# Optimization experiments

Measured on AMD Instinct MI355X. Metric: run time of the kernel, lower is better.

Reference implementation:

```python
import jax, jax.numpy as jnp
import numpy as np

B, S = 64, 256
F, H, V = 512, 2048, 32000
PAD = 0
LN_EPS = 1e-5


def setup_inputs() -> dict:
    key = jax.random.key(0)
    ks = jax.random.split(key, 10)
    inputs = jax.random.randint(ks[0], (B, S), 0, V, dtype=jnp.int64)
    targets = jax.random.randint(ks[1], (B, S), 0, V, dtype=jnp.int64)
    # parameters (kaiming-ish / torch-default-ish scales)
    see = jax.random.normal(ks[2], (2 * F, F), jnp.float32) * (2.0 / (2 * F)) ** 0.5
    bias = jnp.zeros((F,), jnp.float32)
    W_in = jax.random.normal(ks[3], (H, F), jnp.float32) * (1.0 / F) ** 0.5
    b_in = jnp.zeros((H,), jnp.float32)
    W_out = jax.random.normal(ks[4], (F, H), jnp.float32) * (1.0 / H) ** 0.5
    b_out = jnp.zeros((F,), jnp.float32)
    ln_g = jnp.ones((F,), jnp.float32)
    ln_b = jnp.zeros((F,), jnp.float32)
    emb = jax.random.normal(ks[5], (V, F), jnp.float32)
    return {"inputs": inputs, "targets": targets, "see": see, "bias": bias,
            "W_in": W_in, "b_in": b_in, "W_out": W_out, "b_out": b_out,
            "ln_g": ln_g, "ln_b": ln_b, "emb": emb}


def _layernorm(x, g, b):
    mu = jnp.mean(x, axis=-1, keepdims=True)
    var = jnp.mean((x - mu) ** 2, axis=-1, keepdims=True)
    return (x - mu) * jax.lax.rsqrt(var + LN_EPS) * g + b


def reference(inputs, targets, see, bias, W_in, b_in, W_out, b_out, ln_g, ln_b, emb):
    emb_m = emb.at[PAD].set(0.0)  # padding_idx row is zero
    inv_sqrt_f = 1.0 / (F ** 0.5)

    def step(state, xy):
        idx, tgt = xy                      # [B], [B]
        vecs = emb_m[idx]                  # [B,F]
        gate = jax.nn.sigmoid(jnp.concatenate([vecs, state], axis=-1) @ see + bias)
        cont = state * gate + vecs * (1.0 - gate)
        h = jax.nn.relu(_layernorm(cont, ln_g, ln_b) @ W_in.T + b_in)
        out = h @ W_out.T + b_out          # [B,F]
        logits = (out @ emb_m.T) * inv_sqrt_f  # [B,V]
        logp = jax.nn.log_softmax(logits, axis=-1)
        nll = -jnp.take_along_axis(logp, tgt[:, None], axis=1)[:, 0]
        mask = (tgt != PAD).astype(logits.dtype)
        li = jnp.sum(nll * mask) / jnp.maximum(jnp.sum(mask), 1.0)
        return cont, li

    xs = (inputs.T, targets.T)  # [S,B]
    _, losses = jax.lax.scan(step, jnp.zeros((inputs.shape[0], F), emb.dtype), xs)
    return jnp.mean(losses)
```

## Files before the change

### kernel.cpp

```cpp
#include <hip/hip_runtime.h>
#include <hip/hip_fp8.h>

#define F_DIM 512
#define H_DIM 2048
#define V_DIM 32000
#define B_DIM 64
#define S_DIM 256
#define ROWS (S_DIM*B_DIM)
#define NT_LOG 250
#define SCALE 0.04419417382415922f
#define LSE_OFF 40.0f

typedef __attribute__((ext_vector_type(8))) short  short8;
typedef __attribute__((ext_vector_type(4))) float  floatx4;

static __device__ inline unsigned short f2bf(float x){
  unsigned int u = __float_as_uint(x);
  u += 0x7fffu + ((u >> 16) & 1u);
  return (unsigned short)(u >> 16);
}
static __device__ inline float bf2f(unsigned short u){
  return __uint_as_float(((unsigned int)u) << 16);
}
static __device__ inline unsigned char f2fp8(float x){
  __hip_fp8_e4m3 q(x);
  return q.__x;
}
static __device__ inline int sw8(int row, int col){
  int g = (col >> 3) & 7;
  int chunk = ((g >> 1) ^ ((row >> 1) & 3));
  int lob = (g & 1) ^ ((row >> 3) & 1);
  return (col & ~63) | (chunk << 4) | (lob << 3) | (col & 7);
}
static __device__ inline float wsum(float v){
  #pragma unroll
  for(int m = 32; m > 0; m >>= 1) v += __shfl_xor(v, m);
  return v;
}
static __device__ inline void load_lds16(const void* g, void* l){
  __builtin_amdgcn_global_load_lds((const __attribute__((address_space(1))) void*)g,
                                   (__attribute__((address_space(3))) void*)l, 16, 0, 0);
}

__global__ __launch_bounds__(256) void cast_w(const float* __restrict__ src,
                                              unsigned short* __restrict__ dst, int n){
  int i = blockIdx.x*256 + threadIdx.x;
  int stride = gridDim.x*256;
  for(; i < n; i += stride) dst[i] = f2bf(src[i]);
}
__global__ __launch_bounds__(256) void cast_emb(const float* __restrict__ src,
    unsigned short* __restrict__ dst, unsigned char* __restrict__ d8){
  int i = blockIdx.x*256 + threadIdx.x;
  int stride = gridDim.x*256;
  for(; i < V_DIM*F_DIM; i += stride){
    float v = (i < F_DIM) ? 0.f : src[i];
    dst[i] = f2bf(v);
    int row = i >> 9, col = i & 511;
    d8[(long)row*512 + sw8(row, col)] = f2fp8(v);
  }
}

__global__ __launch_bounds__(256) void prep_see(const float* __restrict__ see,
    unsigned short* __restrict__ TT, unsigned char* __restrict__ B8){
  int n = blockIdx.x;
  for(int k = threadIdx.x; k < 512; k += 256){
    TT[n*512 + k] = f2bf(see[(long)k*512 + n]);
    B8[n*512 + k] = f2fp8(see[(long)(512+k)*512 + n]);
  }
}

__global__ __launch_bounds__(256) void gather_vecs(const float* __restrict__ emb,
    const int* __restrict__ inp, unsigned short* __restrict__ V){
  long row = (long)blockIdx.x*4 + (threadIdx.x >> 6);
  int l = threadIdx.x & 63;
  int t = (int)(row >> 6), b = (int)(row & 63);
  int idx = inp[b*S_DIM + t];
  short8 o;
  if (idx == 0){
    #pragma unroll
    for(int i=0;i<8;i++) o[i] = 0;
  } else {
    const float* e = emb + (long)idx*F_DIM + l*8;
    float4 a = *(const float4*)e;
    float4 bq = *(const float4*)(e + 4);
    o[0]=(short)f2bf(a.x); o[1]=(short)f2bf(a.y); o[2]=(short)f2bf(a.z); o[3]=(short)f2bf(a.w);
    o[4]=(short)f2bf(bq.x);o[5]=(short)f2bf(bq.y);o[6]=(short)f2bf(bq.z);o[7]=(short)f2bf(bq.w);
  }
  *(short8*)(V + row*F_DIM + l*8) = o;
}

__global__ __launch_bounds__(512, 1) void recurrence_batch(
    const unsigned int* __restrict__ ZV,
    const unsigned char* __restrict__ W8,
    unsigned short* __restrict__ CONTB)
{
  __shared__ unsigned char stt[2][16][520];

  const int tid = threadIdx.x;
  const int w  = tid >> 6;
  const int l  = tid & 63;
  const int rl = l & 15, rq = l >> 4;
  const int wg = blockIdx.x;
  const int colb = w*64;

  long Bfr[16][4];
  #pragma unroll
  for(int c=0;c<16;c++)
    #pragma unroll
    for(int tl=0;tl<4;tl++)
      Bfr[c][tl] = *(const long*)(W8 + (long)(colb + tl*16 + rl)*512 + c*32 + rq*8);

  float s_old[16];
  #pragma unroll
  for(int i=0;i<16;i++) s_old[i] = 0.f;

  const unsigned int* zbase = ZV + (long)(wg*16 + rq*4)*512 + colb + rl;
  unsigned short* cbase = CONTB + ((long)wg*16 + rq*4)*512 + colb + rl;

  unsigned int zv[16];
  #pragma unroll
  for(int tl=0;tl<4;tl++)
    #pragma unroll
    for(int r=0;r<4;r++)
      zv[tl*4+r] = zbase[(long)r*512 + tl*16];

  for(int t = 0; t < S_DIM; t++){
    unsigned int zvn[16];
    if (t+1 < S_DIM){
      const unsigned int* zp = zbase + (long)(t+1)*64*512;
      #pragma unroll
      for(int tl=0;tl<4;tl++)
        #pragma unroll
        for(int r=0;r<4;r++)
          zvn[tl*4+r] = zp[(long)r*512 + tl*16];
    }

    asm volatile("s_waitcnt lgkmcnt(0)" ::: "memory");
    __builtin_amdgcn_s_barrier();
    asm volatile("" ::: "memory");

    floatx4 acc[4];
    #pragma unroll
    for(int tl=0;tl<4;tl++) acc[tl] = (floatx4)0.f;

    if (t > 0){
      const unsigned char* sb = &stt[(t-1)&1][0][0];
      #pragma unroll
      for(int c=0;c<16;c++){
        long a = *(const long*)(sb + rl*520 + c*32 + rq*8);
        #pragma unroll
        for(int tl=0;tl<4;tl++)
          acc[tl] = __builtin_amdgcn_mfma_f32_16x16x32_fp8_fp8(a, Bfr[c][tl], acc[tl], 0, 0, 0);
      }
    }

    unsigned short* cw = cbase + (long)t*64*512;
    unsigned char* swb = &stt[t&1][0][0] + rq*4*520 + colb + rl;
    #pragma unroll
    for(int tl=0;tl<4;tl++){
      float sv[4];
      #pragma unroll
      for(int r=0;r<4;r++){
        unsigned int p = zv[tl*4+r];
        float z = __uint_as_float(p << 16) + acc[tl][r];
        float v = __uint_as_float(p & 0xffff0000u);
        float e = __expf(-z);
        float g = __builtin_amdgcn_rcpf(1.f + e);
        float s = fmaf(s_old[tl*4+r] - v, g, v);
        s_old[tl*4+r] = s;
        sv[r] = s;
      }
      #pragma unroll
      for(int pr=0; pr<2; pr++){
        unsigned int bfp, f8p;
        asm("v_cvt_pk_bf16_f32 %0, %1, %2" : "=v"(bfp) : "v"(sv[pr*2]), "v"(sv[pr*2+1]));
        asm("v_cvt_pk_fp8_f32 %0, %1, %2"  : "=v"(f8p) : "v"(sv[pr*2]), "v"(sv[pr*2+1]));
        cw[(long)(pr*2)*512   + tl*16] = (unsigned short)(bfp & 0xffffu);
        cw[(long)(pr*2+1)*512 + tl*16] = (unsigned short)(bfp >> 16);
        swb[(pr*2)*520   + tl*16] = (unsigned char)(f8p & 0xffu);
        swb[(pr*2+1)*520 + tl*16] = (unsigned char)((f8p >> 8) & 0xffu);
      }
    }

    if (t+1 < S_DIM){
      #pragma unroll
      for(int i=0;i<16;i++) zv[i] = zvn[i];
    }
  }
}

__global__ __launch_bounds__(256) void ln_kernel(const unsigned short* __restrict__ contb,
    const float* __restrict__ lg, const float* __restrict__ lb,
    unsigned short* __restrict__ xln)
{
  const int wid = threadIdx.x >> 6, l = threadIdx.x & 63;
  const long row = (long)blockIdx.x*4 + wid;
  short8 xv = *(const short8*)(contb + row*F_DIM + l*8);
  float v[8];
  #pragma unroll
  for(int i=0;i<8;i++) v[i] = bf2f((unsigned short)xv[i]);
  float s = 0.f;
  #pragma unroll
  for(int i=0;i<8;i++) s += v[i];
  s = wsum(s);
  float mu = s * (1.f/512.f);
  float q = 0.f;
  #pragma unroll
  for(int i=0;i<8;i++){ float d = v[i]-mu; q += d*d; }
  q = wsum(q);
  float rs = rsqrtf(q*(1.f/512.f) + 1e-5f);
  short8 o;
  #pragma unroll
  for(int i=0;i<8;i++)
    o[i] = (short)f2bf((v[i]-mu)*rs*lg[l*8+i] + lb[l*8+i]);
  *(short8*)(xln + row*F_DIM + l*8) = o;
}

template<int MODE>
__global__ __launch_bounds__(256) void gemm_bt(
    const unsigned short* __restrict__ A,
    const unsigned short* __restrict__ Bm,
    const float* __restrict__ bias,
    unsigned short* __restrict__ C,
    unsigned char* __restrict__ C8,
    const unsigned short* __restrict__ Vsrc,
    unsigned int* __restrict__ ZVout,
    int M, int N, int K, int tiles_m, int tiles_n)
{
  __shared__ short As[128*64];
  __shared__ short Bs[128*64];

  const int bid = blockIdx.x;
  const int mt = bid % tiles_m;
  const int nt = bid / tiles_m;
  const long m0 = (long)mt * 128;
  const long n0 = (long)nt * 128;
  const int tid = threadIdx.x;
  const int l = tid & 63;
  const int wid = tid >> 6;
  const int wr = wid >> 1, wc = wid & 1;
  const int rl = l & 15, rq = l >> 4;

  const short* Ag = (const short*)A + m0 * K;
  const short* Bg = (const short*)Bm + n0 * K;
  const int grow = tid >> 3;
  const int kp = tid & 7;
  const int ksw = (kp ^ (grow & 7)) * 8;

  floatx4 acc[4][4];
  #pragma unroll
  for(int i=0;i<4;i++)
    #pragma unroll
    for(int j=0;j<4;j++) acc[i][j] = (floatx4)0.f;

  for(int k0 = 0; k0 < K; k0 += 64){
    __syncthreads();
    #pragma unroll
    for(int ro = 0; ro < 128; ro += 32){
      load_lds16(Ag + (long)(ro + grow)*K + k0 + ksw, (void*)(As + (ro+grow)*64 + kp*8));
      load_lds16(Bg + (long)(ro + grow)*K + k0 + ksw, (void*)(Bs + (ro+grow)*64 + kp*8));
    }
    __syncthreads();
    #pragma unroll
    for(int kb = 0; kb < 64; kb += 32){
      const int cb = kb >> 3;
      const int cl = ((cb + rq) ^ (rl & 7)) * 8;
      short8 af[4], bfr[4];
      #pragma unroll
      for(int i=0;i<4;i++) af[i]  = *(const short8*)(As + (wr*64 + i*16 + rl)*64 + cl);
      #pragma unroll
      for(int j=0;j<4;j++) bfr[j] = *(const short8*)(Bs + (wc*64 + j*16 + rl)*64 + cl);
      #pragma unroll
      for(int i=0;i<4;i++)
        #pragma unroll
        for(int j=0;j<4;j++)
          acc[i][j] = __builtin_amdgcn_mfma_f32_16x16x32_bf16(af[i], bfr[j], acc[i][j], 0, 0, 0);
    }
  }

  const long mb = m0 + wr*64;
  const long nb = n0 + wc*64;
  #pragma unroll
  for(int j=0;j<4;j++){
    float bj = bias[nb + j*16 + rl];
    #pragma unroll
    for(int i=0;i<4;i++){
      #pragma unroll
      for(int r=0;r<4;r++){
        float v = acc[i][j][r] + bj;
        if (MODE == 0) v = fmaxf(v, 0.f);
        int rowI = (int)(mb + i*16 + rq*4 + r);
        int colI = (int)(nb + j*16 + rl);
        long idx = (long)rowI*N + colI;
        if (MODE == 5){
          ZVout[idx] = ((unsigned)Vsrc[idx] << 16) | (unsigned)f2bf(v);
        } else {
          C[idx] = f2bf(v);
          if (MODE == 4) C8[(long)rowI*512 + sw8(rowI, colI)] = f2fp8(v);
        }
      }
    }
  }
}

__global__ __launch_bounds__(256) void gemm_f8_logits(
    const unsigned char* __restrict__ A8,
    const unsigned char* __restrict__ B8,
    float* __restrict__ part,
    int M, int N, int K, int tiles_m, int tiles_n)
{
  __shared__ unsigned char As8[128*64];
  __shared__ unsigned char Bs8[128*64];
  __shared__ float sm2[2][64][2];

  const int bid = blockIdx.x;
  const int mt = bid % tiles_m;
  const int nt = bid / tiles_m;
  const long m0 = (long)mt * 128;
  const long n0 = (long)nt * 128;
  const int tid = threadIdx.x;
  const int l = tid & 63;
  const int wid = tid >> 6;
  const int wr = wid >> 1, wc = wid & 1;
  const int rl = l & 15, rq = l >> 4;

  const unsigned char* Ag = A8 + m0 * K;
  const unsigned char* Bg = B8 + n0 * K;
  const int grow = tid >> 2;
  const int kp = tid & 3;

  floatx4 acc[4][4];
  #pragma unroll
  for(int i=0;i<4;i++)
    #pragma unroll
    for(int j=0;j<4;j++) acc[i][j] = (floatx4)0.f;

  const int rsw = (rl >> 1) & 3;
  const int rhi = (rl >> 3) & 1;

  for(int k0 = 0; k0 < K; k0 += 64){
    __syncthreads();
    #pragma unroll
    for(int ro = 0; ro < 128; ro += 64){
      load_lds16(Ag + (long)(ro + grow)*K + k0 + kp*16, (void*)(As8 + (ro+grow)*64 + kp*16));
      load_lds16(Bg + (long)(ro + grow)*K + k0 + kp*16, (void*)(Bs8 + (ro+grow)*64 + kp*16));
    }
    __syncthreads();
    #pragma unroll
    for(int kb = 0; kb < 64; kb += 32){
      const int g = (kb >> 3) + rq;
      const int cl = ((((g >> 1) ^ rsw)) << 4) | ((((g & 1) ^ rhi)) << 3);
      long af[4], bfr[4];
      #pragma unroll
      for(int i=0;i<4;i++) af[i]  = *(const long*)(As8 + (wr*64 + i*16 + rl)*64 + cl);
      #pragma unroll
      for(int j=0;j<4;j++) bfr[j] = *(const long*)(Bs8 + (wc*64 + j*16 + rl)*64 + cl);
      #pragma unroll
      for(int i=0;i<4;i++)
        #pragma unroll
        for(int j=0;j<4;j++)
          acc[i][j] = __builtin_amdgcn_mfma_f32_16x16x32_fp8_fp8(af[i], bfr[j], acc[i][j], 0, 0, 0);
    }
  }

  #pragma unroll
  for(int i=0;i<4;i++){
    #pragma unroll
    for(int r=0;r<4;r++){
      float sv = 0.f;
      #pragma unroll
      for(int j=0;j<4;j++) sv += __expf(acc[i][j][r]*SCALE - LSE_OFF);
      #pragma unroll
      for(int d=1; d<16; d<<=1) sv += __shfl_xor(sv, d);
      if (rl == 0) sm2[wr][i*16 + rq*4 + r][wc] = sv;
    }
  }
  __syncthreads();
  if (tid < 128){
    int wr2 = tid >> 6, rowl = tid & 63;
    part[(m0 + wr2*64 + rowl)*tiles_n + nt] = sm2[wr2][rowl][0] + sm2[wr2][rowl][1];
  }
}

__global__ __launch_bounds__(256) void tlogit_kernel(const unsigned short* __restrict__ outb,
    const unsigned short* __restrict__ embb, const int* __restrict__ tgt,
    float* __restrict__ TL)
{
  long gw = (long)blockIdx.x*4 + (threadIdx.x >> 6);
  int l = threadIdx.x & 63;
  int t = (int)(gw >> 6), b = (int)(gw & 63);
  int tg = tgt[b*S_DIM + t];
  const unsigned short* o = outb + gw*F_DIM;
  const unsigned short* e = embb + (long)tg*F_DIM;
  short8 ov = *(const short8*)(o + l*8);
  short8 ev = *(const short8*)(e + l*8);
  float s = 0.f;
  #pragma unroll
  for(int i=0;i<8;i++) s += bf2f((unsigned short)ov[i]) * bf2f((unsigned short)ev[i]);
  s = wsum(s);
  if (l == 0) TL[gw] = s * SCALE;
}

__global__ __launch_bounds__(256) void lse_kernel(const float* __restrict__ part,
    const float* __restrict__ TL, float* __restrict__ nll)
{
  long row = (long)blockIdx.x*4 + (threadIdx.x >> 6);
  int l = threadIdx.x & 63;
  float S = 0.f;
  for(int c = l; c < NT_LOG; c += 64)
    S += part[row*NT_LOG + c];
  S = wsum(S);
  if (l == 0) nll[row] = (LSE_OFF + logf(S)) - TL[row];
}

__global__ __launch_bounds__(256) void loss_kernel(const float* __restrict__ nll,
    const int* __restrict__ tgt, float* __restrict__ out)
{
  int t = threadIdx.x;
  float s = 0.f; int cnt = 0;
  for(int b = 0; b < B_DIM; b++){
    int v = tgt[b*S_DIM + t];
    if (v != 0){ s += nll[(long)t*B_DIM + b]; cnt++; }
  }
  float li = s / fmaxf((float)cnt, 1.f);
  li = wsum(li);
  __shared__ float red[4];
  if ((t & 63) == 0) red[t >> 6] = li;
  __syncthreads();
  if (t == 0) out[0] = (red[0]+red[1]+red[2]+red[3]) * (1.f/256.f);
}

extern "C" void kernel_launch(void* const* d_in, const int* in_sizes, int n_in,
                              void* d_out, int out_size, void* d_ws, size_t ws_size,
                              hipStream_t stream)
{
  const int*   inp   = (const int*)d_in[0];
  const int*   tgt   = (const int*)d_in[1];
  const float* see   = (const float*)d_in[2];
  const float* bias  = (const float*)d_in[3];
  const float* W_in  = (const float*)d_in[4];
  const float* b_in  = (const float*)d_in[5];
  const float* W_out = (const float*)d_in[6];
  const float* b_out = (const float*)d_in[7];
  const float* ln_g  = (const float*)d_in[8];
  const float* ln_b  = (const float*)d_in[9];
  const float* emb   = (const float*)d_in[10];

  char* p = (char*)d_ws;
  unsigned short* CONTB= (unsigned short*)p; p += (size_t)ROWS*F_DIM*2;
  unsigned short* Hb   = (unsigned short*)p; p += (size_t)ROWS*H_DIM*2;
  unsigned short* OUTb = (unsigned short*)p; p += (size_t)ROWS*F_DIM*2;
  unsigned short* EMBb = (unsigned short*)p; p += (size_t)V_DIM*F_DIM*2;
  unsigned char* EMB8  = (unsigned char*)p;  p += (size_t)V_DIM*F_DIM;
  unsigned short* WINb = (unsigned short*)p; p += (size_t)H_DIM*F_DIM*2;
  unsigned short* WOUTb= (unsigned short*)p; p += (size_t)F_DIM*H_DIM*2;
  float* TL            = (float*)p;          p += (size_t)ROWS*4;
  float* NLL           = (float*)p;          p += (size_t)ROWS*4;
  unsigned short* VECSb= (unsigned short*)p; p += (size_t)ROWS*F_DIM*2;
  unsigned int* ZV     = (unsigned int*)p;   p += (size_t)ROWS*F_DIM*4;
  unsigned short* SEETT= (unsigned short*)p; p += (size_t)F_DIM*F_DIM*2;
  unsigned char* SEEB8 = (unsigned char*)p;  p += (size_t)F_DIM*F_DIM;
  unsigned short* XLN  = (unsigned short*)ZV;
  unsigned char* OUT8  = (unsigned char*)VECSb;
  float* PART          = (float*)Hb;

  cast_emb<<<4096, 256, 0, stream>>>(emb, EMBb, EMB8);
  cast_w<<<2048, 256, 0, stream>>>(W_in,  WINb,  H_DIM*F_DIM);
  cast_w<<<2048, 256, 0, stream>>>(W_out, WOUTb, F_DIM*H_DIM);
  prep_see<<<512, 256, 0, stream>>>(see, SEETT, SEEB8);
  gather_vecs<<<ROWS/4, 256, 0, stream>>>(emb, inp, VECSb);

  gemm_bt<5><<<128*4, 256, 0, stream>>>(VECSb, SEETT, bias, nullptr, nullptr,
                                        VECSb, ZV, ROWS, F_DIM, F_DIM, 128, 4);

  recurrence_batch<<<4, 512, 0, stream>>>(ZV, SEEB8, CONTB);

  ln_kernel<<<ROWS/4, 256, 0, stream>>>(CONTB, ln_g, ln_b, XLN);
  gemm_bt<0><<<128*16, 256, 0, stream>>>(XLN,  WINb,  b_in,  Hb,   nullptr,
                                         nullptr, nullptr, ROWS, H_DIM, F_DIM, 128, 16);
  gemm_bt<4><<<128*4,  256, 0, stream>>>(Hb,   WOUTb, b_out, OUTb, OUT8,
                                         nullptr, nullptr, ROWS, F_DIM, H_DIM, 128, 4);
  tlogit_kernel<<<ROWS/4, 256, 0, stream>>>(OUTb, EMBb, tgt, TL);
  gemm_f8_logits<<<128*NT_LOG, 256, 0, stream>>>(OUT8, EMB8, PART, ROWS, V_DIM, F_DIM, 128, NT_LOG);
  lse_kernel<<<ROWS/4, 256, 0, stream>>>(PART, TL, NLL);
  loss_kernel<<<1, 256, 0, stream>>>(NLL, tgt, (float*)d_out);
}
```

Measured before the change: 1.336 ms.

## Double-buffer LDS tiles in fp8 logits GEMM to overlap loads with MFMA

The fp8 logits GEMM now keeps two LDS buffers per operand and prefetches two K-tiles ahead with direct-to-LDS loads. Each iteration reads all of its fragments into registers, then issues the next prefetch before running the MFMAs, using explicit vmcnt/lgkmcnt waits, barriers and raised wave priority. The goal is to hide global memory latency behind the matrix math. In exchange, LDS use doubles and the hand-written waitcnt and barrier sequence must stay correct.

```diff
diff --git a/kernel.cpp b/kernel.cpp
--- a/kernel.cpp
+++ b/kernel.cpp
@@ -309,8 +309,8 @@
     float* __restrict__ part,
     int M, int N, int K, int tiles_m, int tiles_n)
 {
-  __shared__ unsigned char As8[128*64];
-  __shared__ unsigned char Bs8[128*64];
+  __shared__ unsigned char As8[2][128*64];
+  __shared__ unsigned char Bs8[2][128*64];
   __shared__ float sm2[2][64][2];
 
   const int bid = blockIdx.x;
@@ -338,30 +338,55 @@
   const int rsw = (rl >> 1) & 3;
   const int rhi = (rl >> 3) & 1;
 
-  for(int k0 = 0; k0 < K; k0 += 64){
-    __syncthreads();
-    #pragma unroll
-    for(int ro = 0; ro < 128; ro += 64){
-      load_lds16(Ag + (long)(ro + grow)*K + k0 + kp*16, (void*)(As8 + (ro+grow)*64 + kp*16));
-      load_lds16(Bg + (long)(ro + grow)*K + k0 + kp*16, (void*)(Bs8 + (ro+grow)*64 + kp*16));
-    }
-    __syncthreads();
-    #pragma unroll
-    for(int kb = 0; kb < 64; kb += 32){
-      const int g = (kb >> 3) + rq;
+  const int nkt = K >> 6;
+
+  #define STAGE_F8(bb, kk) do {                                               \
+    const long kof = (long)(kk)*64 + kp*16;                                   \
+    load_lds16(Ag + (long)grow*K       + kof, (void*)(&As8[bb][grow*64       + kp*16])); \
+    load_lds16(Ag + (long)(64+grow)*K  + kof, (void*)(&As8[bb][(64+grow)*64  + kp*16])); \
+    load_lds16(Bg + (long)grow*K       + kof, (void*)(&Bs8[bb][grow*64       + kp*16])); \
+    load_lds16(Bg + (long)(64+grow)*K  + kof, (void*)(&Bs8[bb][(64+grow)*64  + kp*16])); \
+  } while(0)
+
+  STAGE_F8(0, 0);
+  STAGE_F8(1, 1);
+
+  for(int t = 0; t < nkt; t++){
+    if (t < nkt-1) asm volatile("s_waitcnt vmcnt(4)" ::: "memory");
+    else           asm volatile("s_waitcnt vmcnt(0)" ::: "memory");
+    __builtin_amdgcn_s_barrier();
+    __builtin_amdgcn_sched_barrier(0);
+
+    const unsigned char* Abuf = &As8[t & 1][0];
+    const unsigned char* Bbuf = &Bs8[t & 1][0];
+    long af[2][4], bfr[2][4];
+    #pragma unroll
+    for(int kb = 0; kb < 2; kb++){
+      const int g = (kb << 2) + rq;
       const int cl = ((((g >> 1) ^ rsw)) << 4) | ((((g & 1) ^ rhi)) << 3);
-      long af[4], bfr[4];
-      #pragma unroll
-      for(int i=0;i<4;i++) af[i]  = *(const long*)(As8 + (wr*64 + i*16 + rl)*64 + cl);
-      #pragma unroll
-      for(int j=0;j<4;j++) bfr[j] = *(const long*)(Bs8 + (wc*64 + j*16 + rl)*64 + cl);
+      #pragma unroll
+      for(int i=0;i<4;i++) af[kb][i]  = *(const long*)(Abuf + (wr*64 + i*16 + rl)*64 + cl);
+      #pragma unroll
+      for(int j=0;j<4;j++) bfr[kb][j] = *(const long*)(Bbuf + (wc*64 + j*16 + rl)*64 + cl);
+    }
+    asm volatile("s_waitcnt lgkmcnt(0)" ::: "memory");
+    __builtin_amdgcn_sched_barrier(0);
+    __builtin_amdgcn_s_barrier();
+    __builtin_amdgcn_sched_barrier(0);
+
+    if (t+2 < nkt) STAGE_F8(t & 1, t+2);
+
+    __builtin_amdgcn_s_setprio(1);
+    #pragma unroll
+    for(int kb = 0; kb < 2; kb++)
       #pragma unroll
       for(int i=0;i<4;i++)
         #pragma unroll
         for(int j=0;j<4;j++)
-          acc[i][j] = __builtin_amdgcn_mfma_f32_16x16x32_fp8_fp8(af[i], bfr[j], acc[i][j], 0, 0, 0);
-    }
-  }
+          acc[i][j] = __builtin_amdgcn_mfma_f32_16x16x32_fp8_fp8(af[kb][i], bfr[kb][j], acc[i][j], 0, 0, 0);
+    __builtin_amdgcn_s_setprio(0);
+  }
+  #undef STAGE_F8
 
   #pragma unroll
   for(int i=0;i<4;i++){
```

Result: faster. 1.269 ms (-5.0%).
